# Optimization experiments

Hardware: AMD Instinct MI355X
Metric: run time of the kernel (lower is better)

The kernel has to match this reference:

```python
import jax, jax.numpy as jnp
import numpy as np

N = 100000
F_IN = 128
E = 1_600_000
NEG_SLOPE = 0.2  # PyG GATConv default negative_slope


def _seg_sum(v, idx, n):
    return jax.ops.segment_sum(v, idx, num_segments=n)


def gcn_conv(x, W, b, src, dst, n):
    # PyG GCNConv: D^{-1/2} (A + I) D^{-1/2} X W + b (self loops already in src/dst)
    h = x @ W
    deg = _seg_sum(jnp.ones(src.shape, h.dtype), dst, n)
    dinv = jnp.where(deg > 0, jax.lax.rsqrt(deg), 0.0)
    norm = dinv[src] * dinv[dst]  # [E]
    return _seg_sum(h[src] * norm[:, None], dst, n) + b


def gat_conv(x, W, a_src, a_dst, b, src, dst, n, heads, out_ch):
    # PyG GATConv (concat=True), eval mode (dropout inactive)
    h = (x @ W).reshape(n, heads, out_ch)          # [n,H,C]
    s = jnp.einsum('nhc,hc->nh', h, a_src)          # per-node src score
    t = jnp.einsum('nhc,hc->nh', h, a_dst)          # per-node dst score
    e = jax.nn.leaky_relu(s[src] + t[dst], NEG_SLOPE)  # [E,H]
    m = jax.ops.segment_max(e, dst, num_segments=n)    # stable segment softmax
    m = jnp.where(jnp.isfinite(m), m, 0.0)
    p = jnp.exp(e - m[dst])
    denom = _seg_sum(p, dst, n)
    alpha = p / (denom[dst] + 1e-16)                 # [E,H]
    out = _seg_sum(h[src] * alpha[:, :, None], dst, n)  # [n,H,C]
    return out.reshape(n, heads * out_ch) + b


def setup_inputs():
    key = jax.random.key(0)
    ks = jax.random.split(key, 24)
    x = jax.random.normal(ks[0], (N, F_IN), jnp.float32) * 0.1
    half = N // 2
    # one-hot user/item type flags read by forward (x[:,0]==1 / x[:,1]==1)
    x = x.at[:, 0].set(0.0).at[:, 1].set(0.0)
    x = x.at[:half, 0].set(1.0).at[half:, 1].set(1.0)
    src = jax.random.randint(ks[1], (E,), 0, N, dtype=jnp.int32)
    dst = jax.random.randint(ks[2], (E,), 0, N, dtype=jnp.int32)
    edge_index = jnp.stack([src, dst])

    def p(k, shape):
        return jax.random.normal(k, shape, jnp.float32) * 0.1

    inp = {"x": x, "edge_index": edge_index,
           "gcn_w": p(ks[3], (F_IN, 16)), "gcn_b": jnp.zeros((16,), jnp.float32)}
    dims = [(16, 16, 8), (128, 16, 8), (128, 16, 8), (128, 2, 1)]
    for i, (fi, fo, h) in enumerate(dims, start=1):
        inp[f"g{i}_w"] = p(ks[3 + 4 * i], (fi, h * fo))
        inp[f"g{i}_as"] = p(ks[4 + 4 * i], (h, fo))
        inp[f"g{i}_ad"] = p(ks[5 + 4 * i], (h, fo))
        inp[f"g{i}_b"] = jnp.zeros((h * fo,), jnp.float32)
    return inp


def reference(x, edge_index, gcn_w, gcn_b,
              g1_w, g1_as, g1_ad, g1_b,
              g2_w, g2_as, g2_ad, g2_b,
              g3_w, g3_as, g3_ad, g3_b,
              g4_w, g4_as, g4_ad, g4_b):
    n = x.shape[0]
    loops = jnp.arange(n, dtype=edge_index.dtype)  # self loops (added by GCN/GAT layers)
    src = jnp.concatenate([edge_index[0], loops])
    dst = jnp.concatenate([edge_index[1], loops])
    h = jax.nn.elu(gcn_conv(x, gcn_w, gcn_b, src, dst, n))
    h = jax.nn.elu(gat_conv(h, g1_w, g1_as, g1_ad, g1_b, src, dst, n, 8, 16))
    h = jax.nn.elu(gat_conv(h, g2_w, g2_as, g2_ad, g2_b, src, dst, n, 8, 16))
    h = jax.nn.elu(gat_conv(h, g3_w, g3_as, g3_ad, g3_b, src, dst, n, 8, 16))
    h = jax.nn.elu(gat_conv(h, g4_w, g4_as, g4_ad, g4_b, src, dst, n, 1, 2))  # [n,2]
    half = n // 2  # users are rows [:half], items rows [half:]
    out = jnp.concatenate([h[:half], h[half:]], axis=1)  # [half,4]
    return jax.nn.log_softmax(out, axis=1)
```

## Files before the change

### kernel.cpp

```cpp
#include <hip/hip_runtime.h>
#include <cstddef>
#include <cstdint>

#define NN 100000
#define NPAD 100032
#define NE 1600000
#define ET (NE + NN)
#define ETP_MAX (ET + 8 * NN)
#define HALFN (NN / 2)
#define NEG_SLOPE 0.2f
#define SCB 1024
#define RP 8
#define RNODES (NN / RP)
#define CHUNK 8192

typedef __attribute__((ext_vector_type(8))) short short8v;
typedef __attribute__((ext_vector_type(4))) float float4v;
typedef __attribute__((ext_vector_type(2))) float float2v;

__device__ __forceinline__ float lrelu(float x) { return x > 0.f ? x : NEG_SLOPE * x; }

__device__ __forceinline__ uint16_t f2bf(float f) {
  uint32_t u = __float_as_uint(f);
  uint32_t r = u + 0x7fffu + ((u >> 16) & 1u);
  return (uint16_t)(r >> 16);
}
__device__ __forceinline__ float bflo(uint32_t u) { return __uint_as_float(u << 16); }
__device__ __forceinline__ float bfhi(uint32_t u) { return __uint_as_float(u & 0xffff0000u); }

template<int K, int M>
__launch_bounds__(256)
__global__ void gemm4_kernel(const float* __restrict__ X, const float* __restrict__ W,
                             float* __restrict__ Y, int n) {
  constexpr int CG = M / 4;
  constexpr int RG = 256 / CG;
  constexpr int RPT = 2;
  constexpr int RT = RG * RPT;
  constexpr int KP = K + 1;
  __shared__ __align__(16) float sW[K * M];
  __shared__ float sX[RT * KP];
  for (int i = threadIdx.x; i < K * M; i += 256) sW[i] = W[i];
  const int jg = threadIdx.x % CG;
  const int rg = threadIdx.x / CG;
  const int r0 = rg * RPT;
  for (int base = blockIdx.x * RT; base < n; base += gridDim.x * RT) {
    __syncthreads();
    const int nrows = (n - base) < RT ? (n - base) : RT;
    for (int i = threadIdx.x; i < nrows * K; i += 256) {
      int r = i / K, c = i - r * K;
      sX[r * KP + c] = X[(size_t)base * K + i];
    }
    __syncthreads();
    float acc[RPT][4];
    #pragma unroll
    for (int rr = 0; rr < RPT; ++rr) acc[rr][0] = acc[rr][1] = acc[rr][2] = acc[rr][3] = 0.f;
    #pragma unroll 4
    for (int k = 0; k < K; ++k) {
      const float4 w = *(const float4*)&sW[k * M + jg * 4];
      #pragma unroll
      for (int rr = 0; rr < RPT; ++rr) {
        const float xv = sX[(r0 + rr) * KP + k];
        acc[rr][0] = fmaf(xv, w.x, acc[rr][0]);
        acc[rr][1] = fmaf(xv, w.y, acc[rr][1]);
        acc[rr][2] = fmaf(xv, w.z, acc[rr][2]);
        acc[rr][3] = fmaf(xv, w.w, acc[rr][3]);
      }
    }
    #pragma unroll
    for (int rr = 0; rr < RPT; ++rr) {
      if (r0 + rr < nrows) {
        float4 o = make_float4(acc[rr][0], acc[rr][1], acc[rr][2], acc[rr][3]);
        *(float4*)&Y[(size_t)(base + r0 + rr) * M + jg * 4] = o;
      }
    }
  }
}

__launch_bounds__(256)
__global__ void wpack_all_kernel(const float* __restrict__ W0, const float* __restrict__ W1,
                                 const float* __restrict__ W2, uint16_t* __restrict__ wp) {
  int tid = blockIdx.x * 256 + threadIdx.x;
  const float* W; int Kreal, KB, base, t;
  if (tid < 512)       { W = W0; Kreal = 16;  KB = 1; base = 0;     t = tid; }
  else if (tid < 2560) { W = W1; Kreal = 128; KB = 4; base = 4096;  t = tid - 512; }
  else if (tid < 4608) { W = W2; Kreal = 128; KB = 4; base = 20480; t = tid - 2560; }
  else return;
  int lane = t & 63;
  int ctkb = t >> 6;
  int kb = ctkb % KB, ct = ctkb / KB;
  int nc = ct * 16 + (lane & 15);
  int k0 = kb * 32 + (lane >> 4) * 8;
  uint16_t v[8];
  #pragma unroll
  for (int j = 0; j < 8; ++j) {
    int k = k0 + j;
    v[j] = (k < Kreal) ? f2bf(W[(size_t)k * 128 + nc]) : (uint16_t)0;
  }
  ushort4 o0, o1;
  o0.x = v[0]; o0.y = v[1]; o0.z = v[2]; o0.w = v[3];
  o1.x = v[4]; o1.y = v[5]; o1.z = v[6]; o1.w = v[7];
  *(ushort4*)&wp[(size_t)base + (size_t)t * 8] = o0;
  *(ushort4*)&wp[(size_t)base + (size_t)t * 8 + 4] = o1;
}

template<int KB, int XS>
__launch_bounds__(256)
__global__ void gemm_mfma_kernel(const uint16_t* __restrict__ X,
                                 const uint16_t* __restrict__ wp,
                                 const float* __restrict__ aS, const float* __restrict__ aD,
                                 uint16_t* __restrict__ Y,
                                 float* __restrict__ S, float* __restrict__ T, int n) {
  __shared__ float sC[4][16 * 136];
  const int wv = threadIdx.x >> 6;
  const int lane = threadIdx.x & 63;
  const int rowbase = blockIdx.x * 64 + wv * 16;
  int arow = rowbase + (lane & 15);
  if (arow >= n) arow = n - 1;
  const uint16_t* xp = X + (size_t)arow * XS + ((lane >> 4) * 8);
  short8v a[KB];
  #pragma unroll
  for (int kb = 0; kb < KB; ++kb) a[kb] = *(const short8v*)(xp + kb * 32);
  #pragma unroll
  for (int ct = 0; ct < 8; ++ct) {
    float4v acc = {0.f, 0.f, 0.f, 0.f};
    #pragma unroll
    for (int kb = 0; kb < KB; ++kb) {
      short8v b = *(const short8v*)&wp[(size_t)((ct * KB + kb) * 64 + lane) * 8];
      acc = __builtin_amdgcn_mfma_f32_16x16x32_bf16(a[kb], b, acc, 0, 0, 0);
    }
    #pragma unroll
    for (int r = 0; r < 4; ++r)
      sC[wv][((lane >> 4) * 4 + r) * 136 + ct * 16 + (lane & 15)] = acc[r];
  }
  #pragma unroll
  for (int t = 0; t < 4; ++t) {
    int idx = t * 64 + lane;
    int row = idx >> 4;
    int c8 = idx & 15;
    const float* pr = &sC[wv][row * 136 + c8 * 8];
    float4 lo = *(const float4*)pr;
    float4 hi = *(const float4*)(pr + 4);
    uint4 o;
    o.x = (uint32_t)f2bf(lo.x) | ((uint32_t)f2bf(lo.y) << 16);
    o.y = (uint32_t)f2bf(lo.z) | ((uint32_t)f2bf(lo.w) << 16);
    o.z = (uint32_t)f2bf(hi.x) | ((uint32_t)f2bf(hi.y) << 16);
    o.w = (uint32_t)f2bf(hi.z) | ((uint32_t)f2bf(hi.w) << 16);
    *(uint4*)&Y[(size_t)(rowbase + row) * 128 + c8 * 8] = o;
  }
  {
    int r = lane & 15;
    int hg = lane >> 4;
    int node = rowbase + r;
    if (node < n) {
      #pragma unroll
      for (int hh = 0; hh < 2; ++hh) {
        int h = hg * 2 + hh;
        float sv = 0.f, tv = 0.f;
        #pragma unroll
        for (int c = 0; c < 16; ++c) {
          float v = sC[wv][r * 136 + h * 16 + c];
          sv = fmaf(v, aS[h * 16 + c], sv);
          tv = fmaf(v, aD[h * 16 + c], tv);
        }
        S[(size_t)node * 8 + h] = sv;
        T[(size_t)node * 8 + h] = tv;
      }
    }
  }
}

template<int K, int ROWS>
__launch_bounds__(256)
__global__ void gemm_s2_kernel(const uint16_t* __restrict__ Xb, const float* __restrict__ W,
                               const float* __restrict__ aS, const float* __restrict__ aD,
                               float* __restrict__ Y, float* __restrict__ S,
                               float* __restrict__ T, int n) {
  constexpr int KP = K + 1;
  __shared__ float sW[K * 2];
  __shared__ float sX[ROWS * KP];
  if (blockIdx.x == 0 && threadIdx.x == 0) {
    S[NN] = -1e30f; T[NN] = 0.f;
    Y[(size_t)NN * 2] = 0.f; Y[(size_t)NN * 2 + 1] = 0.f;
  }
  for (int i = threadIdx.x; i < K * 2; i += 256) sW[i] = W[i];
  const float as0 = aS[0], as1 = aS[1], ad0 = aD[0], ad1 = aD[1];
  for (int base = blockIdx.x * ROWS; base < n; base += gridDim.x * ROWS) {
    __syncthreads();
    const int nrows = (n - base) < ROWS ? (n - base) : ROWS;
    for (int i = threadIdx.x; i < nrows * (K / 4); i += 256) {
      int r = i / (K / 4), c = i - r * (K / 4);
      uint2 u = *(const uint2*)&Xb[(size_t)(base + r) * K + c * 4];
      sX[r * KP + c * 4 + 0] = bflo(u.x);
      sX[r * KP + c * 4 + 1] = bfhi(u.x);
      sX[r * KP + c * 4 + 2] = bflo(u.y);
      sX[r * KP + c * 4 + 3] = bfhi(u.y);
    }
    __syncthreads();
    for (int r = threadIdx.x; r < nrows; r += 256) {
      float a0 = 0.f, a1 = 0.f;
      #pragma unroll 4
      for (int k = 0; k < K; ++k) {
        float xv = sX[r * KP + k];
        a0 = fmaf(xv, sW[k * 2], a0);
        a1 = fmaf(xv, sW[k * 2 + 1], a1);
      }
      int node = base + r;
      float2 o; o.x = a0; o.y = a1;
      *(float2*)&Y[(size_t)node * 2] = o;
      S[node] = a0 * as0 + a1 * as1;
      T[node] = a0 * ad0 + a1 * ad1;
    }
  }
}

__launch_bounds__(256)
__global__ void rank_kernel(const int* __restrict__ edst, int* __restrict__ cursor,
                            int* __restrict__ rank) {
  int e = blockIdx.x * 256 + threadIdx.x;
  if (e >= ET) return;
  int dn = e < NE ? edst[e] : e - NE;
  rank[e] = atomicAdd(&cursor[dn], 1);
}

__device__ __forceinline__ int pad4i(int d) { return (d + 3) & ~3; }

__launch_bounds__(256)
__global__ void scan1_kernel(const int* __restrict__ degi, int* __restrict__ rowptr,
                             int* __restrict__ bsums) {
  __shared__ int sd[256];
  int t = threadIdx.x;
  int base = blockIdx.x * SCB + t * 4;
  int v0 = base + 0 < NN ? pad4i(degi[base + 0]) : 0;
  int v1 = base + 1 < NN ? pad4i(degi[base + 1]) : 0;
  int v2 = base + 2 < NN ? pad4i(degi[base + 2]) : 0;
  int v3 = base + 3 < NN ? pad4i(degi[base + 3]) : 0;
  int s = v0 + v1 + v2 + v3;
  sd[t] = s;
  __syncthreads();
  for (int off = 1; off < 256; off <<= 1) {
    int x = (t >= off) ? sd[t - off] : 0;
    __syncthreads();
    sd[t] += x;
    __syncthreads();
  }
  int excl = sd[t] - s;
  if (t == 255) bsums[blockIdx.x] = sd[255];
  if (base + 0 < NN) rowptr[base + 0] = excl;
  excl += v0;
  if (base + 1 < NN) rowptr[base + 1] = excl;
  excl += v1;
  if (base + 2 < NN) rowptr[base + 2] = excl;
  excl += v2;
  if (base + 3 < NN) rowptr[base + 3] = excl;
}

__launch_bounds__(256)
__global__ void scan2_kernel(int* __restrict__ bsums, int nb) {
  __shared__ int sd[256];
  int t = threadIdx.x;
  int v = t < nb ? bsums[t] : 0;
  sd[t] = v;
  __syncthreads();
  for (int off = 1; off < 256; off <<= 1) {
    int x = (t >= off) ? sd[t - off] : 0;
    __syncthreads();
    sd[t] += x;
    __syncthreads();
  }
  if (t < nb) bsums[t] = sd[t] - v;
  if (t == nb - 1) bsums[nb] = sd[t];
}

__launch_bounds__(256)
__global__ void scan3_kernel(int* __restrict__ rowptr, const int* __restrict__ bsums, int nb,
                             const int* __restrict__ deg, float* __restrict__ dinv,
                             float* __restrict__ S8, float* __restrict__ T8,
                             int* __restrict__ csr) {
  int i = blockIdx.x * 256 + threadIdx.x;
  if (i == 0) {
    rowptr[NN] = bsums[nb];
    dinv[NN] = 0.f;
    #pragma unroll
    for (int h = 0; h < 8; ++h) {
      S8[(size_t)NN * 8 + h] = -1e30f;
      T8[(size_t)NN * 8 + h] = 0.f;
    }
  }
  if (i >= NN) return;
  int rp = rowptr[i] + bsums[i / SCB];
  rowptr[i] = rp;
  int dg = deg[i];
  dinv[i] = dg > 0 ? rsqrtf((float)dg) : 0.f;
  int pe = rp + pad4i(dg);
  for (int e = rp + dg; e < pe; ++e) csr[e] = NN;
}

__launch_bounds__(256)
__global__ void scatter_part_kernel(const int* __restrict__ esrc, const int* __restrict__ edst,
                                    const int* __restrict__ rowptr, const int* __restrict__ rank,
                                    int* __restrict__ csr_src) {
  int p = blockIdx.x & (RP - 1);
  int c = blockIdx.x >> 3;
  int lo = p * RNODES, hi = lo + RNODES;
  int e0 = c * CHUNK;
  int e1 = e0 + CHUNK < ET ? e0 + CHUNK : ET;
  for (int e = e0 + threadIdx.x; e < e1; e += 256) {
    int dn = e < NE ? edst[e] : e - NE;
    if (dn >= lo && dn < hi) {
      int sn = e < NE ? esrc[e] : e - NE;
      csr_src[rowptr[dn] + rank[e]] = sn;
    }
  }
}

__launch_bounds__(256)
__global__ void fused_gat_kernel(const int* __restrict__ rowptr, const int* __restrict__ csr,
                                 const float* __restrict__ S, const float* __restrict__ T,
                                 const uint16_t* __restrict__ Hm, const float* __restrict__ bias,
                                 uint16_t* __restrict__ Outb) {
  const int lane = threadIdx.x & 63;
  const int d = (blockIdx.x * 256 + threadIdx.x) >> 6;
  if (d >= NN) return;
  const int rs = rowptr[d];
  const int deg = rowptr[d + 1] - rs;
  const int deg8 = deg & ~7;
  const int eg = lane >> 4;
  const int cl = lane & 15;
  const int hp = cl >> 1;
  const float Th = T[(size_t)d * 8 + hp];
  const char* sb = (const char*)S;
  const char* hb = (const char*)Hm;
  float m = -1e38f;
  float s = 0.f;
  float2v A0 = {0.f, 0.f}, A1 = {0.f, 0.f}, A2 = {0.f, 0.f}, A3 = {0.f, 0.f};
  const uint32_t clo = (uint32_t)(cl << 4);
  const uint32_t hpo = (uint32_t)(hp << 2);
  int iA = rs + eg;
  int snA = csr[iA];
  int snB = csr[iA + 4];
  for (int l0 = 0; l0 < deg8; l0 += 8) {
    int snA2 = csr[iA + 8];
    int snB2 = csr[iA + 12];
    uint4 uA = *(const uint4*)(hb + (((uint32_t)snA << 8) + clo));
    uint4 uB = *(const uint4*)(hb + (((uint32_t)snB << 8) + clo));
    float svA = *(const float*)(sb + (((uint32_t)snA << 5) + hpo));
    float svB = *(const float*)(sb + (((uint32_t)snB << 5) + hpo));
    iA += 8;
    float eA = lrelu(svA + Th);
    float eB = lrelu(svB + Th);
    float nm = fmaxf(m, fmaxf(eA, eB));
    if (nm > m) {
      float sc = __expf(m - nm);
      float2v scv = {sc, sc};
      s *= sc;
      A0 *= scv; A1 *= scv; A2 *= scv; A3 *= scv;
      m = nm;
    }
    float pA = __expf(eA - m);
    float pB = __expf(eB - m);
    s += pA + pB;
    float2v ppA = {pA, pA}, ppB = {pB, pB};
    A0 = ppA * (float2v){bflo(uA.x), bfhi(uA.x)} + A0;
    A1 = ppA * (float2v){bflo(uA.y), bfhi(uA.y)} + A1;
    A2 = ppA * (float2v){bflo(uA.z), bfhi(uA.z)} + A2;
    A3 = ppA * (float2v){bflo(uA.w), bfhi(uA.w)} + A3;
    A0 = ppB * (float2v){bflo(uB.x), bfhi(uB.x)} + A0;
    A1 = ppB * (float2v){bflo(uB.y), bfhi(uB.y)} + A1;
    A2 = ppB * (float2v){bflo(uB.z), bfhi(uB.z)} + A2;
    A3 = ppB * (float2v){bflo(uB.w), bfhi(uB.w)} + A3;
    snA = snA2; snB = snB2;
  }
  if (deg & 4) {
    uint4 uA = *(const uint4*)(hb + (((uint32_t)snA << 8) + clo));
    float svA = *(const float*)(sb + (((uint32_t)snA << 5) + hpo));
    float eA = lrelu(svA + Th);
    float nm = fmaxf(m, eA);
    if (nm > m) {
      float sc = __expf(m - nm);
      float2v scv = {sc, sc};
      s *= sc;
      A0 *= scv; A1 *= scv; A2 *= scv; A3 *= scv;
      m = nm;
    }
    float pA = __expf(eA - m);
    s += pA;
    float2v ppA = {pA, pA};
    A0 = ppA * (float2v){bflo(uA.x), bfhi(uA.x)} + A0;
    A1 = ppA * (float2v){bflo(uA.y), bfhi(uA.y)} + A1;
    A2 = ppA * (float2v){bflo(uA.z), bfhi(uA.z)} + A2;
    A3 = ppA * (float2v){bflo(uA.w), bfhi(uA.w)} + A3;
  }
  #pragma unroll
  for (int mask = 16; mask <= 32; mask <<= 1) {
    float om = __shfl_xor(m, mask);
    float os = __shfl_xor(s, mask);
    float o0x = __shfl_xor(A0.x, mask), o0y = __shfl_xor(A0.y, mask);
    float o1x = __shfl_xor(A1.x, mask), o1y = __shfl_xor(A1.y, mask);
    float o2x = __shfl_xor(A2.x, mask), o2y = __shfl_xor(A2.y, mask);
    float o3x = __shfl_xor(A3.x, mask), o3y = __shfl_xor(A3.y, mask);
    float nm = fmaxf(m, om);
    float s1 = __expf(m - nm), s2 = __expf(om - nm);
    s = s * s1 + os * s2;
    A0.x = A0.x * s1 + o0x * s2; A0.y = A0.y * s1 + o0y * s2;
    A1.x = A1.x * s1 + o1x * s2; A1.y = A1.y * s1 + o1y * s2;
    A2.x = A2.x * s1 + o2x * s2; A2.y = A2.y * s1 + o2y * s2;
    A3.x = A3.x * s1 + o3x * s2; A3.y = A3.y * s1 + o3y * s2;
    m = nm;
  }
  {
    float2v Blo = (eg & 1) ? A1 : A0;
    float2v Bhi = (eg & 1) ? A3 : A2;
    float2v B = (eg & 2) ? Bhi : Blo;
    const float inv = 1.f / (s + 1e-16f);
    float2 b = *(const float2*)&bias[cl * 8 + eg * 2];
    float v0 = fmaf(B.x, inv, b.x);
    float v1 = fmaf(B.y, inv, b.y);
    v0 = v0 > 0.f ? v0 : expm1f(v0);
    v1 = v1 > 0.f ? v1 : expm1f(v1);
    uint32_t o = (uint32_t)f2bf(v0) | ((uint32_t)f2bf(v1) << 16);
    *(uint32_t*)&Outb[(size_t)d * 128 + cl * 8 + eg * 2] = o;
  }
}

__launch_bounds__(256)
__global__ void fused_gat1_kernel(const int* __restrict__ rowptr, const int* __restrict__ csr,
                                  const float* __restrict__ S, const float* __restrict__ T,
                                  const float* __restrict__ Hm2, const float* __restrict__ bias,
                                  float* __restrict__ Out) {
  int lane = threadIdx.x & 63;
  int sub = lane >> 4, l16 = lane & 15;
  int d = ((blockIdx.x * 256 + threadIdx.x) >> 6) * 4 + sub;
  if (d >= NN) return;
  int rs = rowptr[d], deg = rowptr[d + 1] - rs;
  float Td = T[d];
  float m = -1e38f, sAcc = 0.f, a0 = 0.f, a1 = 0.f;
  for (int l = l16; l < deg; l += 16) {
    int sn = csr[rs + l];
    float2 hv = *(const float2*)&Hm2[(size_t)sn * 2];
    float sv = S[sn];
    float e = lrelu(sv + Td);
    float nm = fmaxf(m, e);
    if (e > m) {
      float sc = __expf(m - nm);
      sAcc *= sc; a0 *= sc; a1 *= sc; m = nm;
    }
    float p = __expf(e - m);
    sAcc += p;
    a0 = fmaf(p, hv.x, a0);
    a1 = fmaf(p, hv.y, a1);
  }
  #pragma unroll
  for (int mask = 1; mask <= 8; mask <<= 1) {
    float om = __shfl_xor(m, mask);
    float os = __shfl_xor(sAcc, mask);
    float oa0 = __shfl_xor(a0, mask);
    float oa1 = __shfl_xor(a1, mask);
    float nm = fmaxf(m, om);
    float s1 = __expf(m - nm), s2 = __expf(om - nm);
    sAcc = sAcc * s1 + os * s2;
    a0 = a0 * s1 + oa0 * s2;
    a1 = a1 * s1 + oa1 * s2;
    m = nm;
  }
  if (l16 == 0) {
    float inv = 1.f / (sAcc + 1e-16f);
    float v0 = fmaf(a0, inv, bias[0]);
    float v1 = fmaf(a1, inv, bias[1]);
    v0 = v0 > 0.f ? v0 : expm1f(v0);
    v1 = v1 > 0.f ? v1 : expm1f(v1);
    float2 o; o.x = v0; o.y = v1;
    *(float2*)&Out[(size_t)d * 2] = o;
  }
}

__launch_bounds__(256)
__global__ void gcn_pull_kernel(const int* __restrict__ rowptr, const int* __restrict__ csr_src,
                                const float* __restrict__ dinv, const float* __restrict__ Hm,
                                const float* __restrict__ bias, uint16_t* __restrict__ Outb) {
  int d = blockIdx.x * 16 + threadIdx.x / 16;
  if (d >= NN) return;
  int f = threadIdx.x & 15;
  int rs = rowptr[d], re = rowptr[d + 1];
  float acc = 0.f;
  int j = rs;
  for (; j + 4 <= re; j += 4) {
    int s0 = csr_src[j], s1 = csr_src[j + 1], s2 = csr_src[j + 2], s3 = csr_src[j + 3];
    float d0 = dinv[s0], d1 = dinv[s1], d2 = dinv[s2], d3 = dinv[s3];
    float h0 = Hm[(size_t)s0 * 16 + f], h1 = Hm[(size_t)s1 * 16 + f];
    float h2 = Hm[(size_t)s2 * 16 + f], h3 = Hm[(size_t)s3 * 16 + f];
    acc = fmaf(d0, h0, acc); acc = fmaf(d1, h1, acc);
    acc = fmaf(d2, h2, acc); acc = fmaf(d3, h3, acc);
  }
  for (; j < re; ++j) {
    int sn = csr_src[j];
    acc = fmaf(dinv[sn], Hm[(size_t)sn * 16 + f], acc);
  }
  float v = acc * dinv[d] + bias[f];
  v = v > 0.f ? v : expm1f(v);
  Outb[(size_t)d * 32 + f] = f2bf(v);
  Outb[(size_t)d * 32 + 16 + f] = 0;
}

__launch_bounds__(256)
__global__ void final_kernel(const float* __restrict__ A, float* __restrict__ Out) {
  int i = blockIdx.x * 256 + threadIdx.x;
  if (i >= HALFN) return;
  float v0 = A[(size_t)i * 2 + 0];
  float v1 = A[(size_t)i * 2 + 1];
  float v2 = A[(size_t)(i + HALFN) * 2 + 0];
  float v3 = A[(size_t)(i + HALFN) * 2 + 1];
  float m = fmaxf(fmaxf(v0, v1), fmaxf(v2, v3));
  float e0 = __expf(v0 - m), e1 = __expf(v1 - m), e2 = __expf(v2 - m), e3 = __expf(v3 - m);
  float l = logf(e0 + e1 + e2 + e3) + m;
  Out[(size_t)i * 4 + 0] = v0 - l;
  Out[(size_t)i * 4 + 1] = v1 - l;
  Out[(size_t)i * 4 + 2] = v2 - l;
  Out[(size_t)i * 4 + 3] = v3 - l;
}

extern "C" void kernel_launch(void* const* d_in, const int* in_sizes, int n_in,
                              void* d_out, int out_size, void* d_ws, size_t ws_size,
                              hipStream_t stream) {
  const float* x     = (const float*)d_in[0];
  const int*   eidx  = (const int*)d_in[1];
  const int*   esrc  = eidx;
  const int*   edst  = eidx + NE;
  const float* gcn_w = (const float*)d_in[2];
  const float* gcn_b = (const float*)d_in[3];

  char* ws = (char*)d_ws;
  uint16_t* hbf    = (uint16_t*)(ws + 0);
  uint16_t* bufAb  = (uint16_t*)(ws + 25700000);
  uint16_t* gcnHbf = (uint16_t*)(ws + 51400000);
  float*    bufB   = (float*)   (ws + 57900000);
  float*    bufC   = (float*)   (ws + 64400000);
  float*    Sb     = (float*)   (ws + 65300000);
  float*    Tb     = (float*)   (ws + 68600000);
  uint16_t* wpck   = (uint16_t*)(ws + 71900000);
  int*      rowptr = (int*)     (ws + 151900000);
  int*      cursor = (int*)     (ws + 152300008);
  int*      csr    = (int*)     (ws + 152700008);
  float*    dinv   = (float*)   (ws + 162700008);
  int*      bsums  = (int*)     (ws + 163100016);
  int*      rank   = (int*)     (ws + 163100528);
  uint16_t* w0p    = wpck;
  uint16_t* w1p    = wpck + 4096;
  uint16_t* w2p    = wpck + 20480;

  constexpr int NB_SCAN = (NN + SCB - 1) / SCB;

  hipMemsetAsync(cursor, 0, (size_t)NN * 4, stream);
  rank_kernel<<<(ET + 255) / 256, 256, 0, stream>>>(edst, cursor, rank);
  scan1_kernel<<<NB_SCAN, 256, 0, stream>>>(cursor, rowptr, bsums);
  scan2_kernel<<<1, 256, 0, stream>>>(bsums, NB_SCAN);
  scan3_kernel<<<(NN + 256) / 256, 256, 0, stream>>>(rowptr, bsums, NB_SCAN,
                                                     cursor, dinv, Sb, Tb, csr);
  {
    int nch = (ET + CHUNK - 1) / CHUNK;
    scatter_part_kernel<<<nch * RP, 256, 0, stream>>>(esrc, edst, rowptr, rank, csr);
  }
  wpack_all_kernel<<<18, 256, 0, stream>>>((const float*)d_in[4], (const float*)d_in[8],
                                           (const float*)d_in[12], wpck);

  {
    int tiles = (NN + 127) / 128;
    if (tiles > 4096) tiles = 4096;
    gemm4_kernel<128, 16><<<tiles, 256, 0, stream>>>(x, gcn_w, bufB, NN);
  }
  gcn_pull_kernel<<<(NN + 15) / 16, 256, 0, stream>>>(rowptr, csr, dinv, bufB, gcn_b, gcnHbf);

  gemm_mfma_kernel<1, 32><<<NPAD / 64, 256, 0, stream>>>(
      gcnHbf, w0p, (const float*)d_in[5], (const float*)d_in[6], hbf, Sb, Tb, NN);
  fused_gat_kernel<<<(NN * 64 + 255) / 256, 256, 0, stream>>>(
      rowptr, csr, Sb, Tb, hbf, (const float*)d_in[7], bufAb);

  gemm_mfma_kernel<4, 128><<<NPAD / 64, 256, 0, stream>>>(
      bufAb, w1p, (const float*)d_in[9], (const float*)d_in[10], hbf, Sb, Tb, NN);
  fused_gat_kernel<<<(NN * 64 + 255) / 256, 256, 0, stream>>>(
      rowptr, csr, Sb, Tb, hbf, (const float*)d_in[11], bufAb);

  gemm_mfma_kernel<4, 128><<<NPAD / 64, 256, 0, stream>>>(
      bufAb, w2p, (const float*)d_in[13], (const float*)d_in[14], hbf, Sb, Tb, NN);
  fused_gat_kernel<<<(NN * 64 + 255) / 256, 256, 0, stream>>>(
      rowptr, csr, Sb, Tb, hbf, (const float*)d_in[15], bufAb);

  {
    int tiles = (NN + 127) / 128;
    if (tiles > 2048) tiles = 2048;
    gemm_s2_kernel<128, 128><<<tiles, 256, 0, stream>>>(
        bufAb, (const float*)d_in[16], (const float*)d_in[17], (const float*)d_in[18],
        bufB, Sb, Tb, NN);
    fused_gat1_kernel<<<(NN * 16 + 255) / 256, 256, 0, stream>>>(
        rowptr, csr, Sb, Tb, bufB, (const float*)d_in[19], bufC);
  }

  final_kernel<<<(HALFN + 255) / 256, 256, 0, stream>>>(bufC, (float*)d_out);
}
```

Measured before the change: 503.2 us.

## Build CSR with partitioned degree atomics and store GCN features in bf16

```diff
diff --git a/kernel.cpp b/kernel.cpp
--- a/kernel.cpp
+++ b/kernel.cpp
@@ -12,7 +12,7 @@
 #define SCB 1024
 #define RP 8
 #define RNODES (NN / RP)
-#define CHUNK 8192
+#define CHUNK 16384
 
 typedef __attribute__((ext_vector_type(8))) short short8v;
 typedef __attribute__((ext_vector_type(4))) float float4v;
@@ -27,11 +27,12 @@
 }
 __device__ __forceinline__ float bflo(uint32_t u) { return __uint_as_float(u << 16); }
 __device__ __forceinline__ float bfhi(uint32_t u) { return __uint_as_float(u & 0xffff0000u); }
+__device__ __forceinline__ float bfs(uint16_t u) { return __uint_as_float((uint32_t)u << 16); }
 
 template<int K, int M>
 __launch_bounds__(256)
-__global__ void gemm4_kernel(const float* __restrict__ X, const float* __restrict__ W,
-                             float* __restrict__ Y, int n) {
+__global__ void gemm4b_kernel(const float* __restrict__ X, const float* __restrict__ W,
+                              uint16_t* __restrict__ Y, int n) {
   constexpr int CG = M / 4;
   constexpr int RG = 256 / CG;
   constexpr int RPT = 2;
@@ -39,6 +40,8 @@
   constexpr int KP = K + 1;
   __shared__ __align__(16) float sW[K * M];
   __shared__ float sX[RT * KP];
+  if (blockIdx.x == 0 && threadIdx.x < M)
+    Y[(size_t)n * M + threadIdx.x] = 0;
   for (int i = threadIdx.x; i < K * M; i += 256) sW[i] = W[i];
   const int jg = threadIdx.x % CG;
   const int rg = threadIdx.x / CG;
@@ -69,8 +72,10 @@
     #pragma unroll
     for (int rr = 0; rr < RPT; ++rr) {
       if (r0 + rr < nrows) {
-        float4 o = make_float4(acc[rr][0], acc[rr][1], acc[rr][2], acc[rr][3]);
-        *(float4*)&Y[(size_t)(base + r0 + rr) * M + jg * 4] = o;
+        ushort4 o;
+        o.x = f2bf(acc[rr][0]); o.y = f2bf(acc[rr][1]);
+        o.z = f2bf(acc[rr][2]); o.w = f2bf(acc[rr][3]);
+        *(ushort4*)&Y[(size_t)(base + r0 + rr) * M + jg * 4] = o;
       }
     }
   }
@@ -214,12 +219,16 @@
 }
 
 __launch_bounds__(256)
-__global__ void rank_kernel(const int* __restrict__ edst, int* __restrict__ cursor,
-                            int* __restrict__ rank) {
-  int e = blockIdx.x * 256 + threadIdx.x;
-  if (e >= ET) return;
-  int dn = e < NE ? edst[e] : e - NE;
-  rank[e] = atomicAdd(&cursor[dn], 1);
+__global__ void deg_part_kernel(const int* __restrict__ edst, int* __restrict__ degi) {
+  int p = blockIdx.x & (RP - 1);
+  int c = blockIdx.x >> 3;
+  int lo = p * RNODES, hi = lo + RNODES;
+  int e0 = c * CHUNK;
+  int e1 = e0 + CHUNK < ET ? e0 + CHUNK : ET;
+  for (int e = e0 + threadIdx.x; e < e1; e += 256) {
+    int dn = e < NE ? edst[e] : e - NE;
+    if (dn >= lo && dn < hi) atomicAdd(&degi[dn], 1);
+  }
 }
 
 __device__ __forceinline__ int pad4i(int d) { return (d + 3) & ~3; }
@@ -297,7 +306,7 @@
 
 __launch_bounds__(256)
 __global__ void scatter_part_kernel(const int* __restrict__ esrc, const int* __restrict__ edst,
-                                    const int* __restrict__ rowptr, const int* __restrict__ rank,
+                                    const int* __restrict__ rowptr, int* __restrict__ cur2,
                                     int* __restrict__ csr_src) {
   int p = blockIdx.x & (RP - 1);
   int c = blockIdx.x >> 3;
@@ -308,7 +317,8 @@
     int dn = e < NE ? edst[e] : e - NE;
     if (dn >= lo && dn < hi) {
       int sn = e < NE ? esrc[e] : e - NE;
-      csr_src[rowptr[dn] + rank[e]] = sn;
+      int slot = rowptr[dn] + atomicAdd(&cur2[dn], 1);
+      csr_src[slot] = sn;
     }
   }
 }
@@ -475,7 +485,7 @@
 
 __launch_bounds__(256)
 __global__ void gcn_pull_kernel(const int* __restrict__ rowptr, const int* __restrict__ csr_src,
-                                const float* __restrict__ dinv, const float* __restrict__ Hm,
+                                const float* __restrict__ dinv, const uint16_t* __restrict__ Hm,
                                 const float* __restrict__ bias, uint16_t* __restrict__ Outb) {
   int d = blockIdx.x * 16 + threadIdx.x / 16;
   if (d >= NN) return;
@@ -486,14 +496,14 @@
   for (; j + 4 <= re; j += 4) {
     int s0 = csr_src[j], s1 = csr_src[j + 1], s2 = csr_src[j + 2], s3 = csr_src[j + 3];
     float d0 = dinv[s0], d1 = dinv[s1], d2 = dinv[s2], d3 = dinv[s3];
-    float h0 = Hm[(size_t)s0 * 16 + f], h1 = Hm[(size_t)s1 * 16 + f];
-    float h2 = Hm[(size_t)s2 * 16 + f], h3 = Hm[(size_t)s3 * 16 + f];
+    float h0 = bfs(Hm[(size_t)s0 * 16 + f]), h1 = bfs(Hm[(size_t)s1 * 16 + f]);
+    float h2 = bfs(Hm[(size_t)s2 * 16 + f]), h3 = bfs(Hm[(size_t)s3 * 16 + f]);
     acc = fmaf(d0, h0, acc); acc = fmaf(d1, h1, acc);
     acc = fmaf(d2, h2, acc); acc = fmaf(d3, h3, acc);
   }
   for (; j < re; ++j) {
     int sn = csr_src[j];
-    acc = fmaf(dinv[sn], Hm[(size_t)sn * 16 + f], acc);
+    acc = fmaf(dinv[sn], bfs(Hm[(size_t)sn * 16 + f]), acc);
   }
   float v = acc * dinv[d] + bias[f];
   v = v > 0.f ? v : expm1f(v);
@@ -539,35 +549,34 @@
   uint16_t* wpck   = (uint16_t*)(ws + 71900000);
   int*      rowptr = (int*)     (ws + 151900000);
   int*      cursor = (int*)     (ws + 152300008);
-  int*      csr    = (int*)     (ws + 152700008);
-  float*    dinv   = (float*)   (ws + 162700008);
-  int*      bsums  = (int*)     (ws + 163100016);
-  int*      rank   = (int*)     (ws + 163100528);
+  int*      cur2   = (int*)     (ws + 152700008);
+  int*      csr    = (int*)     (ws + 153100008);
+  float*    dinv   = (float*)   (ws + 163500016);
+  int*      bsums  = (int*)     (ws + 163900024);
   uint16_t* w0p    = wpck;
   uint16_t* w1p    = wpck + 4096;
   uint16_t* w2p    = wpck + 20480;
 
   constexpr int NB_SCAN = (NN + SCB - 1) / SCB;
-
-  hipMemsetAsync(cursor, 0, (size_t)NN * 4, stream);
-  rank_kernel<<<(ET + 255) / 256, 256, 0, stream>>>(edst, cursor, rank);
+  const int nch = (ET + CHUNK - 1) / CHUNK;
+
+  hipMemsetAsync(cursor, 0, (size_t)NN * 8, stream);
+  deg_part_kernel<<<nch * RP, 256, 0, stream>>>(edst, cursor);
   scan1_kernel<<<NB_SCAN, 256, 0, stream>>>(cursor, rowptr, bsums);
   scan2_kernel<<<1, 256, 0, stream>>>(bsums, NB_SCAN);
   scan3_kernel<<<(NN + 256) / 256, 256, 0, stream>>>(rowptr, bsums, NB_SCAN,
                                                      cursor, dinv, Sb, Tb, csr);
-  {
-    int nch = (ET + CHUNK - 1) / CHUNK;
-    scatter_part_kernel<<<nch * RP, 256, 0, stream>>>(esrc, edst, rowptr, rank, csr);
-  }
+  scatter_part_kernel<<<nch * RP, 256, 0, stream>>>(esrc, edst, rowptr, cur2, csr);
   wpack_all_kernel<<<18, 256, 0, stream>>>((const float*)d_in[4], (const float*)d_in[8],
                                            (const float*)d_in[12], wpck);
 
   {
     int tiles = (NN + 127) / 128;
     if (tiles > 4096) tiles = 4096;
-    gemm4_kernel<128, 16><<<tiles, 256, 0, stream>>>(x, gcn_w, bufB, NN);
-  }
-  gcn_pull_kernel<<<(NN + 15) / 16, 256, 0, stream>>>(rowptr, csr, dinv, bufB, gcn_b, gcnHbf);
+    gemm4b_kernel<128, 16><<<tiles, 256, 0, stream>>>(x, gcn_w, (uint16_t*)bufB, NN);
+  }
+  gcn_pull_kernel<<<(NN + 15) / 16, 256, 0, stream>>>(rowptr, csr, dinv,
+                                                      (const uint16_t*)bufB, gcn_b, gcnHbf);
 
   gemm_mfma_kernel<1, 32><<<NPAD / 64, 256, 0, stream>>>(
       gcnHbf, w0p, (const float*)d_in[5], (const float*)d_in[6], hbf, Sb, Tb, NN);
```

Measured after the change: 532.6 us. 1.06x slower.
